# Optimization experiments

Hardware: AMD Instinct MI355X
Metric: run time of the kernel (lower is better)

The kernel has to match this reference:

```python
import jax, jax.numpy as jnp
import numpy as np

C = 512
NUM_GROUPS = 32
EPS = 1e-6


def group_norm(x, gamma, beta):
    # x: [B, C, H, W]
    B, Cc, H, W = x.shape
    xg = x.reshape(B, NUM_GROUPS, Cc // NUM_GROUPS, H, W)
    mean = xg.mean(axis=(2, 3, 4), keepdims=True)
    var = xg.var(axis=(2, 3, 4), keepdims=True)
    xn = (xg - mean) / jnp.sqrt(var + EPS)
    xn = xn.reshape(B, Cc, H, W)
    return xn * gamma[None, :, None, None] + beta[None, :, None, None]


def conv1x1(x, w, b):
    # w: [out_c, in_c], x: [B, C, H, W]
    return jnp.einsum('oc,bchw->bohw', w, x) + b[None, :, None, None]


def setup_inputs() -> dict:
    key = jax.random.key(0)
    ks = jax.random.split(key, 6)
    B, H, W = 2, 64, 64
    x = jax.random.normal(ks[0], (B, C, H, W), dtype=jnp.float32)
    s = 1.0 / np.sqrt(C)
    wq = jax.random.normal(ks[1], (C, C), dtype=jnp.float32) * s
    wk = jax.random.normal(ks[2], (C, C), dtype=jnp.float32) * s
    wv = jax.random.normal(ks[3], (C, C), dtype=jnp.float32) * s
    wo = jax.random.normal(ks[4], (C, C), dtype=jnp.float32) * s
    bq = jnp.zeros((C,), jnp.float32)
    bk = jnp.zeros((C,), jnp.float32)
    bv = jnp.zeros((C,), jnp.float32)
    bo = jnp.zeros((C,), jnp.float32)
    gamma = jnp.ones((C,), jnp.float32)
    beta = jnp.zeros((C,), jnp.float32)
    return {"x": x, "gamma": gamma, "beta": beta, "wq": wq, "bq": bq,
            "wk": wk, "bk": bk, "wv": wv, "bv": bv, "wo": wo, "bo": bo}


def reference(x, gamma, beta, wq, bq, wk, bk, wv, bv, wo, bo):
    B, Cc, H, W = x.shape
    h = group_norm(x, gamma, beta)
    q = conv1x1(h, wq, bq).reshape(B, Cc, H * W)  # [B, C, N]
    k = conv1x1(h, wk, bk).reshape(B, Cc, H * W)
    v = conv1x1(h, wv, bv).reshape(B, Cc, H * W)
    scale = Cc ** (-0.5)
    # scores a[b,i,j] = sum_c q[b,c,i] * k[b,c,j]
    a = jnp.einsum('bci,bcj->bij', q, k) * scale
    a = jax.nn.softmax(a, axis=2)
    # out[b,c,i] = sum_j v[b,c,j] * a[b,i,j]  (matches bmm(v, a^T))
    o = jnp.einsum('bcj,bij->bci', v, a).reshape(B, Cc, H, W)
    o = conv1x1(o, wo, bo)
    return x + o
```

## Files before the change

kernel.cpp:

```cpp
#include <hip/hip_runtime.h>
#include <stdint.h>

#define NPIX 4096
#define CDIM 512

typedef _Float16 hv8 __attribute__((ext_vector_type(8)));
typedef float f32x4 __attribute__((ext_vector_type(4)));

__device__ __forceinline__ void lds_direct16(const _Float16* g, _Float16* l) {
    __builtin_amdgcn_global_load_lds(
        (const __attribute__((address_space(1))) void*)g,
        (__attribute__((address_space(3))) void*)l, 16, 0, 0);
}

__global__ void cvt_w(const float* __restrict__ s0, const float* __restrict__ s1,
                      const float* __restrict__ s2, const float* __restrict__ s3,
                      _Float16* __restrict__ d0, _Float16* __restrict__ d1,
                      _Float16* __restrict__ d2, _Float16* __restrict__ d3) {
    int i = blockIdx.x * 256 + threadIdx.x;
    d0[i] = (_Float16)s0[i];
    d1[i] = (_Float16)s1[i];
    d2[i] = (_Float16)s2[i];
    d3[i] = (_Float16)s3[i];
}

__global__ void stats_kernel(const float* __restrict__ x, float* __restrict__ stats) {
    int idx = blockIdx.x;
    const float4* base = (const float4*)(x + (long)idx * 16 * NPIX);
    int tid = threadIdx.x;
    float s = 0.f, sq = 0.f;
    for (int it = 0; it < 64; ++it) {
        float4 f = base[it * 256 + tid];
        s  += f.x + f.y + f.z + f.w;
        sq += f.x * f.x + f.y * f.y + f.z * f.z + f.w * f.w;
    }
    __shared__ float rs[256], rq[256];
    rs[tid] = s; rq[tid] = sq;
    __syncthreads();
    for (int st = 128; st > 0; st >>= 1) {
        if (tid < st) { rs[tid] += rs[tid + st]; rq[tid] += rq[tid + st]; }
        __syncthreads();
    }
    if (tid == 0) {
        float mean = rs[0] * (1.0f / 65536.0f);
        float var  = rq[0] * (1.0f / 65536.0f) - mean * mean;
        stats[idx * 2]     = mean;
        stats[idx * 2 + 1] = rsqrtf(var + 1e-6f);
    }
}

__global__ void normT_kernel(const float* __restrict__ x, const float* __restrict__ stats,
                             const float* __restrict__ gamma, const float* __restrict__ beta,
                             _Float16* __restrict__ hT) {
    int b = blockIdx.z, c0 = blockIdx.x * 32, n0 = blockIdx.y * 32;
    int tid = threadIdx.x;
    __shared__ float t[32][33];
    int cl = tid >> 5;
    int nl = tid & 31;
    for (int r = 0; r < 4; ++r)
        t[r * 8 + cl][nl] = x[(long)b * CDIM * NPIX + (long)(c0 + r * 8 + cl) * NPIX + n0 + nl];
    __syncthreads();
    for (int r = 0; r < 4; ++r) {
        int nr = r * 8 + cl;
        int c = c0 + nl;
        float m    = stats[(b * 32 + (c >> 4)) * 2];
        float rstd = stats[(b * 32 + (c >> 4)) * 2 + 1];
        float val = (t[nl][nr] - m) * rstd * gamma[c] + beta[c];
        hT[(long)b * NPIX * CDIM + (long)(n0 + nr) * CDIM + c] = (_Float16)val;
    }
}

template<int EPI>
__launch_bounds__(256, 2)
__global__ void gemm_bt_kernel(const _Float16* __restrict__ A, const _Float16* __restrict__ BT,
                               void* __restrict__ D, const float* __restrict__ bias,
                               const float* __restrict__ resid,
                               int M, int N, int K,
                               long aBatch, long bBatch, long dBatch, long rBatch) {
    const int b = blockIdx.z;
    A  += (long)b * aBatch;
    BT += (long)b * bBatch;
    const int m0 = blockIdx.y * 128;
    const int n0 = blockIdx.x * 128;
    const int tid = threadIdx.x;
    const int l = tid & 63;
    const int w = tid >> 6;
    const int wm = (w >> 1) * 64;
    const int wn = (w & 1) * 64;
    const int lr = l & 15;
    const int lk = l >> 4;
    __shared__ __align__(16) _Float16 As[128 * 32];
    __shared__ __align__(16) _Float16 Bs[128 * 32];
    f32x4 acc[4][4] = {};
    const int nK = K >> 5;
    for (int kt = 0; kt < nK; ++kt) {
        const int kb = kt * 32;
#pragma unroll
        for (int c = 0; c < 2; ++c) {
            int chunk = c * 256 + tid;
            int row = chunk >> 2;
            int k8 = (chunk & 3) * 8;
            _Float16* ldsA = As + (size_t)(c * 256 + (tid & ~63)) * 8;
            _Float16* ldsB = Bs + (size_t)(c * 256 + (tid & ~63)) * 8;
            lds_direct16(A  + (long)(m0 + row) * K + kb + k8, ldsA);
            lds_direct16(BT + (long)(n0 + row) * K + kb + k8, ldsB);
        }
        __syncthreads();
        hv8 af[4], bfr[4];
#pragma unroll
        for (int mi = 0; mi < 4; ++mi)
            af[mi] = *(const hv8*)(As + (size_t)(wm + mi * 16 + lr) * 32 + lk * 8);
#pragma unroll
        for (int ni = 0; ni < 4; ++ni)
            bfr[ni] = *(const hv8*)(Bs + (size_t)(wn + ni * 16 + lr) * 32 + lk * 8);
#pragma unroll
        for (int mi = 0; mi < 4; ++mi)
#pragma unroll
            for (int ni = 0; ni < 4; ++ni)
                acc[mi][ni] = __builtin_amdgcn_mfma_f32_16x16x32_f16(af[mi], bfr[ni], acc[mi][ni], 0, 0, 0);
        __syncthreads();
    }
#pragma unroll
    for (int mi = 0; mi < 4; ++mi)
#pragma unroll
        for (int ni = 0; ni < 4; ++ni)
#pragma unroll
            for (int r = 0; r < 4; ++r) {
                int row = m0 + wm + mi * 16 + lk * 4 + r;
                int col = n0 + wn + ni * 16 + lr;
                float val = acc[mi][ni][r];
                if (EPI == 0) {
                    ((_Float16*)D)[(long)b * dBatch + (long)row * N + col] = (_Float16)(val + bias[col]);
                } else if (EPI == 1) {
                    ((_Float16*)D)[(long)b * dBatch + (long)row * N + col] = (_Float16)(val + bias[row]);
                } else {
                    long idx = (long)row * N + col;
                    ((float*)D)[(long)b * dBatch + idx] =
                        val + bias[row] + resid[(long)b * rBatch + idx];
                }
            }
}

__launch_bounds__(512, 2)
__global__ void attn_kernel(const _Float16* __restrict__ qT, const _Float16* __restrict__ kT,
                            const _Float16* __restrict__ v,
                            _Float16* __restrict__ p0, _Float16* __restrict__ p1,
                            float* __restrict__ lbuf) {
    __shared__ __align__(16) _Float16 Ks[2][32 * 512];
    __shared__ __align__(16) _Float16 Vs[2][512 * 32];
    __shared__ __align__(16) char ps[2][64 * 80];
    __shared__ float red[8][64];
    __shared__ float redt[64];

    const int g = blockIdx.x;
    const int xcd = g & 7;
    const int comb = xcd >> 1;
    const int itile = ((g >> 3) << 1) | (xcd & 1);
    const int batch = comb >> 1;
    const int jhalf = comb & 1;
    const int i0 = itile * 64;
    const int jbase = jhalf * 2048;

    const int tid = threadIdx.x;
    const int l = tid & 63, w = tid >> 6;
    const int lr = l & 15, lk = l >> 4;
    const int iq = w >> 1, jq = w & 1;

    const _Float16* qb = qT + (long)batch * NPIX * CDIM;
    const _Float16* kb = kT + (long)batch * NPIX * CDIM;
    const _Float16* vb = v  + (long)batch * CDIM * NPIX;

    hv8 af[16];
    {
        const _Float16* qr = qb + (long)(i0 + iq * 16 + lr) * CDIM + lk * 8;
#pragma unroll
        for (int kk = 0; kk < 16; ++kk)
            af[kk] = *(const hv8*)(qr + kk * 32);
    }

    f32x4 oacc[4][4] = {};
    float lsum[4] = {};
    hv8 vfA[4], vfB[4];

    const int vrow_lo = l >> 2;
    const int vslot   = (l & 3) ^ (vrow_lo & 3);
    const float scale = 0.044194173824159216f;

#define STAGE(BUF, JT)                                                               \
    {                                                                                \
        const long j0s = (long)jbase + (JT) * 32;                                    \
        _Float16* kd = Ks[BUF]; _Float16* vd = Vs[BUF];                              \
        _Pragma("unroll")                                                            \
        for (int q = 0; q < 4; ++q) {                                                \
            int row = q * 8 + w;                                                     \
            int cc = l ^ (row & 7);                                                  \
            lds_direct16(kb + (j0s + row) * CDIM + cc * 8, kd + row * 512);          \
        }                                                                            \
        _Pragma("unroll")                                                            \
        for (int q = 0; q < 4; ++q) {                                                \
            int r16 = q * 8 + w;                                                     \
            int crow = r16 * 16 + vrow_lo;                                           \
            lds_direct16(vb + (long)crow * NPIX + j0s + vslot * 8, vd + r16 * 512);  \
        }                                                                            \
    }

#define VREAD(DST, CUR)                                                              \
    {                                                                                \
        _Pragma("unroll")                                                            \
        for (int ni = 0; ni < 4; ++ni) {                                             \
            int c = w * 64 + ni * 16 + lr;                                           \
            uint32_t off = (uint32_t)(c * 64) + (((uint32_t)(lk * 16)) ^ ((uint32_t)((c & 3) << 4))); \
            DST[ni] = *(const hv8*)((const char*)Vs[CUR] + off);                     \
        }                                                                            \
    }

#define QKEXP(CUR)                                                                   \
    {                                                                                \
        const char* kbase = (const char*)Ks[CUR];                                    \
        f32x4 sa = {}, sb = {};                                                      \
        const int jj = jq * 16 + lr;                                                 \
        const uint32_t sw = (uint32_t)((jj & 7) << 4);                               \
        _Pragma("unroll")                                                            \
        for (int kk = 0; kk < 8; ++kk) {                                             \
            hv8 b0 = *(const hv8*)(kbase + (((uint32_t)(jj * 1024 + (2 * kk) * 64 + lk * 16)) ^ sw));     \
            sa = __builtin_amdgcn_mfma_f32_16x16x32_f16(af[2 * kk], b0, sa, 0, 0, 0);                     \
            hv8 b1 = *(const hv8*)(kbase + (((uint32_t)(jj * 1024 + (2 * kk + 1) * 64 + lk * 16)) ^ sw)); \
            sb = __builtin_amdgcn_mfma_f32_16x16x32_f16(af[2 * kk + 1], b1, sb, 0, 0, 0);                 \
        }                                                                            \
        sa += sb;                                                                    \
        _Pragma("unroll")                                                            \
        for (int r = 0; r < 4; ++r) {                                                \
            float p = __expf(sa[r] * scale);                                         \
            lsum[r] += p;                                                            \
            int i = iq * 16 + lk * 4 + r;                                            \
            int j2 = jq * 16 + lr;                                                   \
            *(_Float16*)(ps[CUR] + i * 80 + j2 * 2) = (_Float16)p;                   \
        }                                                                            \
    }

#define PVSTEP(PRV, VPREV)                                                           \
    {                                                                                \
        _Pragma("unroll")                                                            \
        for (int mi = 0; mi < 4; ++mi) {                                             \
            int i2 = mi * 16 + lr;                                                   \
            hv8 pa = *(const hv8*)(ps[PRV] + i2 * 80 + lk * 16);                     \
            _Pragma("unroll")                                                        \
            for (int ni = 0; ni < 4; ++ni)                                           \
                oacc[mi][ni] = __builtin_amdgcn_mfma_f32_16x16x32_f16(pa, VPREV[ni], oacc[mi][ni], 0, 0, 0); \
        }                                                                            \
    }

#define ENDBAR()                                                                     \
    __builtin_amdgcn_sched_barrier(0);                                               \
    asm volatile("s_waitcnt vmcnt(0) lgkmcnt(0)" ::: "memory");                      \
    __builtin_amdgcn_s_barrier();                                                    \
    __builtin_amdgcn_sched_barrier(0);

#define STEP(JT, CUR, VCUR, VPREV)                                                   \
    {                                                                                \
        const int cur_ = (CUR);                                                      \
        if ((JT) < 63) STAGE(cur_ ^ 1, (JT) + 1)                                     \
        VREAD(VCUR, cur_)                                                            \
        __builtin_amdgcn_s_setprio(1);                                               \
        QKEXP(cur_)                                                                  \
        PVSTEP(cur_ ^ 1, VPREV)                                                      \
        __builtin_amdgcn_s_setprio(0);                                               \
        ENDBAR()                                                                     \
    }

    STAGE(0, 0)
    __builtin_amdgcn_sched_barrier(0);
    asm volatile("s_waitcnt vmcnt(0)" ::: "memory");
    __builtin_amdgcn_s_barrier();
    __builtin_amdgcn_sched_barrier(0);

    STAGE(1, 1)
    VREAD(vfA, 0)
    QKEXP(0)
    ENDBAR()

    for (int jt = 1; jt < 63; jt += 2) {
        STEP(jt,     1, vfB, vfA)
        STEP(jt + 1, 0, vfA, vfB)
    }
    STEP(63, 1, vfB, vfA)

    PVSTEP(1, vfB)

#pragma unroll
    for (int m = 1; m <= 8; m <<= 1)
#pragma unroll
        for (int r = 0; r < 4; ++r)
            lsum[r] += __shfl_xor(lsum[r], m, 64);
    if (lr == 0)
#pragma unroll
        for (int r = 0; r < 4; ++r)
            red[w][iq * 16 + lk * 4 + r] = lsum[r];
    __syncthreads();
    if (tid < 64) {
        int iq2 = tid >> 4;
        float lv = red[iq2 * 2][tid] + red[iq2 * 2 + 1][tid];
        redt[tid] = 1.0f / lv;
        lbuf[jhalf * 8192 + batch * NPIX + i0 + tid] = lv;
    }
    __syncthreads();

    _Float16* dsth = (jhalf ? p1 : p0) + (long)batch * NPIX * CDIM;
#pragma unroll
    for (int mi = 0; mi < 4; ++mi)
#pragma unroll
        for (int r = 0; r < 4; ++r) {
            int row = mi * 16 + lk * 4 + r;
            float rv = redt[row];
#pragma unroll
            for (int ni = 0; ni < 4; ++ni) {
                int c = w * 64 + ni * 16 + lr;
                dsth[(long)(i0 + row) * CDIM + c] = (_Float16)(oacc[mi][ni][r] * rv);
            }
        }
#undef STEP
#undef ENDBAR
#undef PVSTEP
#undef QKEXP
#undef VREAD
#undef STAGE
}

__global__ void combine_kernel(const _Float16* __restrict__ p0, const _Float16* __restrict__ p1,
                               const float* __restrict__ lbuf, _Float16* __restrict__ out) {
    long g = (long)blockIdx.x * 256 + threadIdx.x;
    long base = g * 8;
    int rowg = (int)(g >> 6);
    float l0 = lbuf[rowg], l1 = lbuf[8192 + rowg];
    float w0 = l0 / (l0 + l1);
    float w1 = 1.0f - w0;
    hv8 a = *(const hv8*)(p0 + base);
    hv8 b = *(const hv8*)(p1 + base);
    hv8 o;
#pragma unroll
    for (int i = 0; i < 8; ++i)
        o[i] = (_Float16)((float)a[i] * w0 + (float)b[i] * w1);
    *(hv8*)(out + base) = o;
}

extern "C" void kernel_launch(void* const* d_in, const int* in_sizes, int n_in,
                              void* d_out, int out_size, void* d_ws, size_t ws_size,
                              hipStream_t stream) {
    const float* x     = (const float*)d_in[0];
    const float* gamma = (const float*)d_in[1];
    const float* beta  = (const float*)d_in[2];
    const float* wq    = (const float*)d_in[3];
    const float* bq    = (const float*)d_in[4];
    const float* wk    = (const float*)d_in[5];
    const float* bk    = (const float*)d_in[6];
    const float* wv    = (const float*)d_in[7];
    const float* bv    = (const float*)d_in[8];
    const float* wo    = (const float*)d_in[9];
    const float* bo    = (const float*)d_in[10];
    float* out = (float*)d_out;

    char* ws = (char*)d_ws;
    float* stats = (float*)ws;
    _Float16* wqb = (_Float16*)(ws + 1024);
    _Float16* wkb = wqb + 262144;
    _Float16* wvb = wkb + 262144;
    _Float16* wob = wvb + 262144;
    _Float16* hT  = wob + 262144;
    const long TSZ = (long)2 * NPIX * CDIM;
    _Float16* qT = hT + TSZ;
    _Float16* kT = qT + TSZ;
    _Float16* vv = kT + TSZ;
    _Float16* oT = vv + TSZ;
    float* lbuf = (float*)(oT + TSZ);

    cvt_w<<<dim3(1024), dim3(256), 0, stream>>>(wq, wk, wv, wo, wqb, wkb, wvb, wob);
    stats_kernel<<<dim3(64), dim3(256), 0, stream>>>(x, stats);
    normT_kernel<<<dim3(16, 128, 2), dim3(256), 0, stream>>>(x, stats, gamma, beta, hT);

    const long NC = (long)NPIX * CDIM;
    gemm_bt_kernel<0><<<dim3(4, 32, 2), dim3(256), 0, stream>>>(
        hT, wqb, (void*)qT, bq, nullptr, NPIX, CDIM, CDIM, NC, 0L, NC, 0L);
    gemm_bt_kernel<0><<<dim3(4, 32, 2), dim3(256), 0, stream>>>(
        hT, wkb, (void*)kT, bk, nullptr, NPIX, CDIM, CDIM, NC, 0L, NC, 0L);
    gemm_bt_kernel<1><<<dim3(32, 4, 2), dim3(256), 0, stream>>>(
        wvb, hT, (void*)vv, bv, nullptr, CDIM, NPIX, CDIM, 0L, NC, NC, 0L);

    attn_kernel<<<dim3(256), dim3(512), 0, stream>>>(qT, kT, vv, oT, hT, lbuf);

    combine_kernel<<<dim3(2048), dim3(256), 0, stream>>>(oT, hT, lbuf, qT);

    gemm_bt_kernel<2><<<dim3(32, 4, 2), dim3(256), 0, stream>>>(
        wob, qT, (void*)out, bo, x, CDIM, NPIX, CDIM, 0L, NC, NC, NC);
}
```

Measured before the change: 198.6 us.

## Shrink attention query tile to 32 and load V fragments directly from global

The attention kernel now handles 32 query rows per block instead of 64, with a 64-wide key tile per step, and launches twice as many blocks. V is no longer staged through LDS; each wave loads its V fragments straight from global into registers one step ahead, and the wait allows 8 outstanding loads. This frees LDS space and removes the V LDS round trip while raising parallelism. In exchange, K/V global traffic per query roughly doubles and V global reads are less coalesced.

```diff
diff --git a/kernel.cpp b/kernel.cpp
--- a/kernel.cpp
+++ b/kernel.cpp
@@ -146,11 +146,10 @@
                             const _Float16* __restrict__ v,
                             _Float16* __restrict__ p0, _Float16* __restrict__ p1,
                             float* __restrict__ lbuf) {
-    __shared__ __align__(16) _Float16 Ks[2][32 * 512];
-    __shared__ __align__(16) _Float16 Vs[2][512 * 32];
-    __shared__ __align__(16) char ps[2][64 * 80];
-    __shared__ float red[8][64];
-    __shared__ float redt[64];
+    __shared__ __align__(16) _Float16 Ks[2][64 * 512];
+    __shared__ __align__(16) char ps[2][32 * 144];
+    __shared__ float red[8][32];
+    __shared__ float redt[32];
 
     const int g = blockIdx.x;
     const int xcd = g & 7;
@@ -158,13 +157,13 @@
     const int itile = ((g >> 3) << 1) | (xcd & 1);
     const int batch = comb >> 1;
     const int jhalf = comb & 1;
-    const int i0 = itile * 64;
+    const int i0 = itile * 32;
     const int jbase = jhalf * 2048;
 
     const int tid = threadIdx.x;
     const int l = tid & 63, w = tid >> 6;
     const int lr = l & 15, lk = l >> 4;
-    const int iq = w >> 1, jq = w & 1;
+    const int iq = w >> 2, jq = w & 3;
 
     const _Float16* qb = qT + (long)batch * NPIX * CDIM;
     const _Float16* kb = kT + (long)batch * NPIX * CDIM;
@@ -178,40 +177,32 @@
             af[kk] = *(const hv8*)(qr + kk * 32);
     }
 
-    f32x4 oacc[4][4] = {};
+    f32x4 oacc[2][4] = {};
     float lsum[4] = {};
-    hv8 vfA[4], vfB[4];
-
-    const int vrow_lo = l >> 2;
-    const int vslot   = (l & 3) ^ (vrow_lo & 3);
+    hv8 vfA[4][2], vfB[4][2];
+
+    const _Float16* vptr = vb + (long)(w * 64 + lr) * NPIX + jbase + lk * 8;
     const float scale = 0.044194173824159216f;
 
 #define STAGE(BUF, JT)                                                               \
     {                                                                                \
-        const long j0s = (long)jbase + (JT) * 32;                                    \
-        _Float16* kd = Ks[BUF]; _Float16* vd = Vs[BUF];                              \
-        _Pragma("unroll")                                                            \
-        for (int q = 0; q < 4; ++q) {                                                \
+        const long j0s = (long)jbase + (JT) * 64;                                    \
+        _Float16* kd = Ks[BUF];                                                      \
+        _Pragma("unroll")                                                            \
+        for (int q = 0; q < 8; ++q) {                                                \
             int row = q * 8 + w;                                                     \
             int cc = l ^ (row & 7);                                                  \
             lds_direct16(kb + (j0s + row) * CDIM + cc * 8, kd + row * 512);          \
         }                                                                            \
-        _Pragma("unroll")                                                            \
-        for (int q = 0; q < 4; ++q) {                                                \
-            int r16 = q * 8 + w;                                                     \
-            int crow = r16 * 16 + vrow_lo;                                           \
-            lds_direct16(vb + (long)crow * NPIX + j0s + vslot * 8, vd + r16 * 512);  \
-        }                                                                            \
-    }
-
-#define VREAD(DST, CUR)                                                              \
-    {                                                                                \
-        _Pragma("unroll")                                                            \
-        for (int ni = 0; ni < 4; ++ni) {                                             \
-            int c = w * 64 + ni * 16 + lr;                                           \
-            uint32_t off = (uint32_t)(c * 64) + (((uint32_t)(lk * 16)) ^ ((uint32_t)((c & 3) << 4))); \
-            DST[ni] = *(const hv8*)((const char*)Vs[CUR] + off);                     \
-        }                                                                            \
+    }
+
+#define VLOAD(VF, JT)                                                                \
+    {                                                                                \
+        _Pragma("unroll")                                                            \
+        for (int ni = 0; ni < 4; ++ni)                                               \
+            _Pragma("unroll")                                                        \
+            for (int jh = 0; jh < 2; ++jh)                                           \
+                VF[ni][jh] = *(const hv8*)(vptr + (long)ni * (16 * NPIX) + (JT) * 64 + jh * 32); \
     }
 
 #define QKEXP(CUR)                                                                   \
@@ -234,57 +225,68 @@
             lsum[r] += p;                                                            \
             int i = iq * 16 + lk * 4 + r;                                            \
             int j2 = jq * 16 + lr;                                                   \
-            *(_Float16*)(ps[CUR] + i * 80 + j2 * 2) = (_Float16)p;                   \
+            *(_Float16*)(ps[CUR] + i * 144 + j2 * 2) = (_Float16)p;                  \
         }                                                                            \
     }
 
-#define PVSTEP(PRV, VPREV)                                                           \
-    {                                                                                \
-        _Pragma("unroll")                                                            \
-        for (int mi = 0; mi < 4; ++mi) {                                             \
-            int i2 = mi * 16 + lr;                                                   \
-            hv8 pa = *(const hv8*)(ps[PRV] + i2 * 80 + lk * 16);                     \
+#define PVSTEP(PRV, VF)                                                              \
+    {                                                                                \
+        _Pragma("unroll")                                                            \
+        for (int jk = 0; jk < 2; ++jk) {                                             \
+            hv8 pa[2];                                                               \
+            _Pragma("unroll")                                                        \
+            for (int mi = 0; mi < 2; ++mi) {                                         \
+                int i2 = mi * 16 + lr;                                               \
+                pa[mi] = *(const hv8*)(ps[PRV] + i2 * 144 + jk * 64 + lk * 16);      \
+            }                                                                        \
             _Pragma("unroll")                                                        \
             for (int ni = 0; ni < 4; ++ni)                                           \
-                oacc[mi][ni] = __builtin_amdgcn_mfma_f32_16x16x32_f16(pa, VPREV[ni], oacc[mi][ni], 0, 0, 0); \
+                _Pragma("unroll")                                                    \
+                for (int mi = 0; mi < 2; ++mi)                                       \
+                    oacc[mi][ni] = __builtin_amdgcn_mfma_f32_16x16x32_f16(pa[mi], VF[ni][jk], oacc[mi][ni], 0, 0, 0); \
         }                                                                            \
     }
 
-#define ENDBAR()                                                                     \
+#define ENDBAR(N)                                                                    \
     __builtin_amdgcn_sched_barrier(0);                                               \
-    asm volatile("s_waitcnt vmcnt(0) lgkmcnt(0)" ::: "memory");                      \
+    asm volatile("s_waitcnt vmcnt(" #N ") lgkmcnt(0)" ::: "memory");                 \
     __builtin_amdgcn_s_barrier();                                                    \
     __builtin_amdgcn_sched_barrier(0);
 
-#define STEP(JT, CUR, VCUR, VPREV)                                                   \
-    {                                                                                \
-        const int cur_ = (CUR);                                                      \
-        if ((JT) < 63) STAGE(cur_ ^ 1, (JT) + 1)                                     \
-        VREAD(VCUR, cur_)                                                            \
+#define STEP(JT, CUR, VF)                                                            \
+    {                                                                                \
+        if ((JT) < 31) STAGE((CUR) ^ 1, (JT) + 1)                                    \
+        __builtin_amdgcn_sched_barrier(0);                                           \
         __builtin_amdgcn_s_setprio(1);                                               \
-        QKEXP(cur_)                                                                  \
-        PVSTEP(cur_ ^ 1, VPREV)                                                      \
+        QKEXP(CUR)                                                                   \
+        PVSTEP((CUR) ^ 1, VF)                                                        \
         __builtin_amdgcn_s_setprio(0);                                               \
-        ENDBAR()                                                                     \
+        if ((JT) < 31) VLOAD(VF, (JT) + 1)                                           \
+        ENDBAR(8)                                                                    \
     }
 
     STAGE(0, 0)
+    VLOAD(vfA, 0)
     __builtin_amdgcn_sched_barrier(0);
-    asm volatile("s_waitcnt vmcnt(0)" ::: "memory");
+    asm volatile("s_waitcnt vmcnt(8)" ::: "memory");
     __builtin_amdgcn_s_barrier();
     __builtin_amdgcn_sched_barrier(0);
 
     STAGE(1, 1)
-    VREAD(vfA, 0)
+    __builtin_amdgcn_s_setprio(1);
     QKEXP(0)
-    ENDBAR()
-
-    for (int jt = 1; jt < 63; jt += 2) {
-        STEP(jt,     1, vfB, vfA)
-        STEP(jt + 1, 0, vfA, vfB)
-    }
-    STEP(63, 1, vfB, vfA)
-
+    __builtin_amdgcn_s_setprio(0);
+    VLOAD(vfB, 1)
+    ENDBAR(8)
+
+    for (int jt = 1; jt < 31; jt += 2) {
+        STEP(jt,     1, vfA)
+        STEP(jt + 1, 0, vfB)
+    }
+    STEP(31, 1, vfA)
+
+    asm volatile("s_waitcnt vmcnt(0)" ::: "memory");
+    __builtin_amdgcn_sched_barrier(0);
     PVSTEP(1, vfB)
 
 #pragma unroll
@@ -297,9 +299,10 @@
         for (int r = 0; r < 4; ++r)
             red[w][iq * 16 + lk * 4 + r] = lsum[r];
     __syncthreads();
-    if (tid < 64) {
-        int iq2 = tid >> 4;
-        float lv = red[iq2 * 2][tid] + red[iq2 * 2 + 1][tid];
+    if (tid < 32) {
+        int iqq = tid >> 4;
+        float lv = red[iqq * 4 + 0][tid] + red[iqq * 4 + 1][tid]
+                 + red[iqq * 4 + 2][tid] + red[iqq * 4 + 3][tid];
         redt[tid] = 1.0f / lv;
         lbuf[jhalf * 8192 + batch * NPIX + i0 + tid] = lv;
     }
@@ -307,7 +310,7 @@
 
     _Float16* dsth = (jhalf ? p1 : p0) + (long)batch * NPIX * CDIM;
 #pragma unroll
-    for (int mi = 0; mi < 4; ++mi)
+    for (int mi = 0; mi < 2; ++mi)
 #pragma unroll
         for (int r = 0; r < 4; ++r) {
             int row = mi * 16 + lk * 4 + r;
@@ -322,7 +325,7 @@
 #undef ENDBAR
 #undef PVSTEP
 #undef QKEXP
-#undef VREAD
+#undef VLOAD
 #undef STAGE
 }
 
@@ -385,7 +388,7 @@
     gemm_bt_kernel<1><<<dim3(32, 4, 2), dim3(256), 0, stream>>>(
         wvb, hT, (void*)vv, bv, nullptr, CDIM, NPIX, CDIM, 0L, NC, NC, 0L);
 
-    attn_kernel<<<dim3(256), dim3(512), 0, stream>>>(qT, kT, vv, oT, hT, lbuf);
+    attn_kernel<<<dim3(512), dim3(512), 0, stream>>>(qT, kT, vv, oT, hT, lbuf);
 
     combine_kernel<<<dim3(2048), dim3(256), 0, stream>>>(oT, hT, lbuf, qT);
 
```

Result: slower. 267.4 us (+34.7%).

## Load V fragments directly from global into registers instead of via LDS

Applied to the files above, without the earlier changes.

Drops the double-buffered V staging in shared memory. Each wave now loads its V MFMA operands straight from global memory into registers at the end of each step, and a partial vmcnt wait lets those loads overlap the barrier and the next step's work. This cuts LDS traffic and footprint, which could raise occupancy and remove the LDS read pass. The cost is uncoalesced 16-byte global loads per lane and a stall on global-load latency just before the next step's PV MFMAs.

```diff
diff --git a/kernel.cpp b/kernel.cpp
--- a/kernel.cpp
+++ b/kernel.cpp
@@ -147,7 +147,6 @@
                             _Float16* __restrict__ p0, _Float16* __restrict__ p1,
                             float* __restrict__ lbuf) {
     __shared__ __align__(16) _Float16 Ks[2][32 * 512];
-    __shared__ __align__(16) _Float16 Vs[2][512 * 32];
     __shared__ __align__(16) char ps[2][64 * 80];
     __shared__ float red[8][64];
     __shared__ float redt[64];
@@ -180,38 +179,28 @@
 
     f32x4 oacc[4][4] = {};
     float lsum[4] = {};
-    hv8 vfA[4], vfB[4];
-
-    const int vrow_lo = l >> 2;
-    const int vslot   = (l & 3) ^ (vrow_lo & 3);
+    hv8 vf[4];
+
+    const _Float16* vptr = vb + (long)(w * 64 + lr) * NPIX + jbase + lk * 8;
     const float scale = 0.044194173824159216f;
 
 #define STAGE(BUF, JT)                                                               \
     {                                                                                \
         const long j0s = (long)jbase + (JT) * 32;                                    \
-        _Float16* kd = Ks[BUF]; _Float16* vd = Vs[BUF];                              \
+        _Float16* kd = Ks[BUF];                                                      \
         _Pragma("unroll")                                                            \
         for (int q = 0; q < 4; ++q) {                                                \
             int row = q * 8 + w;                                                     \
             int cc = l ^ (row & 7);                                                  \
             lds_direct16(kb + (j0s + row) * CDIM + cc * 8, kd + row * 512);          \
         }                                                                            \
-        _Pragma("unroll")                                                            \
-        for (int q = 0; q < 4; ++q) {                                                \
-            int r16 = q * 8 + w;                                                     \
-            int crow = r16 * 16 + vrow_lo;                                           \
-            lds_direct16(vb + (long)crow * NPIX + j0s + vslot * 8, vd + r16 * 512);  \
-        }                                                                            \
-    }
-
-#define VREAD(DST, CUR)                                                              \
-    {                                                                                \
-        _Pragma("unroll")                                                            \
-        for (int ni = 0; ni < 4; ++ni) {                                             \
-            int c = w * 64 + ni * 16 + lr;                                           \
-            uint32_t off = (uint32_t)(c * 64) + (((uint32_t)(lk * 16)) ^ ((uint32_t)((c & 3) << 4))); \
-            DST[ni] = *(const hv8*)((const char*)Vs[CUR] + off);                     \
-        }                                                                            \
+    }
+
+#define VLOAD(JT)                                                                    \
+    {                                                                                \
+        _Pragma("unroll")                                                            \
+        for (int ni = 0; ni < 4; ++ni)                                               \
+            vf[ni] = *(const hv8*)(vptr + (long)ni * (16 * NPIX) + (JT) * 32);       \
     }
 
 #define QKEXP(CUR)                                                                   \
@@ -238,7 +227,7 @@
         }                                                                            \
     }
 
-#define PVSTEP(PRV, VPREV)                                                           \
+#define PVSTEP(PRV)                                                                  \
     {                                                                                \
         _Pragma("unroll")                                                            \
         for (int mi = 0; mi < 4; ++mi) {                                             \
@@ -246,26 +235,27 @@
             hv8 pa = *(const hv8*)(ps[PRV] + i2 * 80 + lk * 16);                     \
             _Pragma("unroll")                                                        \
             for (int ni = 0; ni < 4; ++ni)                                           \
-                oacc[mi][ni] = __builtin_amdgcn_mfma_f32_16x16x32_f16(pa, VPREV[ni], oacc[mi][ni], 0, 0, 0); \
+                oacc[mi][ni] = __builtin_amdgcn_mfma_f32_16x16x32_f16(pa, vf[ni], oacc[mi][ni], 0, 0, 0); \
         }                                                                            \
     }
 
-#define ENDBAR()                                                                     \
+#define ENDBAR(N)                                                                    \
     __builtin_amdgcn_sched_barrier(0);                                               \
-    asm volatile("s_waitcnt vmcnt(0) lgkmcnt(0)" ::: "memory");                      \
+    asm volatile("s_waitcnt vmcnt(" #N ") lgkmcnt(0)" ::: "memory");                 \
     __builtin_amdgcn_s_barrier();                                                    \
     __builtin_amdgcn_sched_barrier(0);
 
-#define STEP(JT, CUR, VCUR, VPREV)                                                   \
-    {                                                                                \
-        const int cur_ = (CUR);                                                      \
-        if ((JT) < 63) STAGE(cur_ ^ 1, (JT) + 1)                                     \
-        VREAD(VCUR, cur_)                                                            \
+#define STEP(JT, CUR)                                                                \
+    {                                                                                \
+        if ((JT) < 63) STAGE((CUR) ^ 1, (JT) + 1)                                    \
+        __builtin_amdgcn_sched_barrier(0);                                           \
         __builtin_amdgcn_s_setprio(1);                                               \
-        QKEXP(cur_)                                                                  \
-        PVSTEP(cur_ ^ 1, VPREV)                                                      \
+        QKEXP(CUR)                                                                   \
+        PVSTEP((CUR) ^ 1)                                                            \
         __builtin_amdgcn_s_setprio(0);                                               \
-        ENDBAR()                                                                     \
+        __builtin_amdgcn_sched_barrier(0);                                           \
+        VLOAD(JT)                                                                    \
+        ENDBAR(4)                                                                    \
     }
 
     STAGE(0, 0)
@@ -275,17 +265,21 @@
     __builtin_amdgcn_sched_barrier(0);
 
     STAGE(1, 1)
-    VREAD(vfA, 0)
+    __builtin_amdgcn_s_setprio(1);
     QKEXP(0)
-    ENDBAR()
+    __builtin_amdgcn_s_setprio(0);
+    VLOAD(0)
+    ENDBAR(4)
 
     for (int jt = 1; jt < 63; jt += 2) {
-        STEP(jt,     1, vfB, vfA)
-        STEP(jt + 1, 0, vfA, vfB)
-    }
-    STEP(63, 1, vfB, vfA)
-
-    PVSTEP(1, vfB)
+        STEP(jt,     1)
+        STEP(jt + 1, 0)
+    }
+    STEP(63, 1)
+
+    asm volatile("s_waitcnt vmcnt(0)" ::: "memory");
+    __builtin_amdgcn_sched_barrier(0);
+    PVSTEP(1)
 
 #pragma unroll
     for (int m = 1; m <= 8; m <<= 1)
@@ -322,7 +316,7 @@
 #undef ENDBAR
 #undef PVSTEP
 #undef QKEXP
-#undef VREAD
+#undef VLOAD
 #undef STAGE
 }
 
```

Result: faster. 191.9 us (-3.3%).
